# Optimization experiments

Measured on AMD Instinct MI355X. Metric: run time of the kernel, lower is better.

The kernel has to match this reference:

```python
import jax, jax.numpy as jnp
import numpy as np

ANNEAL = 0.01

def _tsig(x, temp=ANNEAL):
    # temperature sigmoid with +/-50 clipping as in the torch source
    return jax.nn.sigmoid(jnp.clip(x / temp, -50.0, 50.0))

def setup_inputs() -> dict:
    key = jax.random.key(0)
    k1, k2 = jax.random.split(key)
    N, D = 512, 512
    preds = jax.random.normal(k1, (N, D), dtype=jnp.float32)
    labels = jax.random.randint(k2, (N,), 0, 64, dtype=jnp.int64)
    return {"preds": preds, "labels": labels}

def reference(preds, labels):
    N = preds.shape[0]
    dtype = preds.dtype
    eye = jnp.eye(N, dtype=dtype)
    same = (labels[:, None] == labels[None, :]).astype(dtype)
    I_pos = same * (1.0 - eye)                      # positives excl. self
    sim_mat = preds @ preds.T                       # [N, N]
    # sim_diff[i, j, k] = sim_mat[i, k] - sim_mat[i, j]
    sim_sg = _tsig(sim_mat[:, None, :] - sim_mat[:, :, None]) * (1.0 - eye)[None, :, :]
    sim_all_rk = 1.0 + jnp.sum(sim_sg, axis=-1)     # [N, N]
    # sum_k sim_sg[i,j,k] * I_pos[i,k]
    pos_sum = jnp.einsum('ijk,ik->ij', sim_sg, I_pos)
    sim_pos_rk = eye + I_pos + I_pos * pos_sum      # [N, N]
    n_pos = jnp.sum(I_pos, axis=1) + 1.0            # [N]
    per_anchor = jnp.sum(sim_pos_rk / sim_all_rk, axis=1) / n_pos
    per_anchor = jnp.where(n_pos > 1.0, per_anchor, 0.0)  # skip anchors with no positives
    ap = jnp.sum(per_anchor) / N
    return 1.0 - ap
```

## Files before the change

kernel.cpp:

```cpp
#include <hip/hip_runtime.h>
#include <hip/hip_bf16.h>

#define NN 512

__global__ __launch_bounds__(256) void sap_gemm(const float* __restrict__ P,
                                                float* __restrict__ S) {
    __shared__ float As[32][33];
    __shared__ float Bs[32][33];
    const int t  = threadIdx.x;
    const int tx = t & 15, ty = t >> 4;
    const int i0 = blockIdx.y * 32, j0 = blockIdx.x * 32;

    float acc00 = 0.f, acc01 = 0.f, acc10 = 0.f, acc11 = 0.f;

    const int lr = t >> 3;
    const int lc = (t & 7) * 4;

    for (int kt = 0; kt < NN; kt += 32) {
        float4 a = *(const float4*)&P[(i0 + lr) * NN + kt + lc];
        float4 b = *(const float4*)&P[(j0 + lr) * NN + kt + lc];
        As[lr][lc + 0] = a.x; As[lr][lc + 1] = a.y;
        As[lr][lc + 2] = a.z; As[lr][lc + 3] = a.w;
        Bs[lr][lc + 0] = b.x; Bs[lr][lc + 1] = b.y;
        Bs[lr][lc + 2] = b.z; Bs[lr][lc + 3] = b.w;
        __syncthreads();
#pragma unroll
        for (int kk = 0; kk < 32; kk++) {
            float a0 = As[2 * ty][kk],     a1 = As[2 * ty + 1][kk];
            float b0 = Bs[2 * tx][kk],     b1 = Bs[2 * tx + 1][kk];
            acc00 += a0 * b0; acc01 += a0 * b1;
            acc10 += a1 * b0; acc11 += a1 * b1;
        }
        __syncthreads();
    }
    const int i = i0 + 2 * ty, j = j0 + 2 * tx;
    S[i * NN + j]           = acc00;
    S[i * NN + j + 1]       = acc01;
    S[(i + 1) * NN + j]     = acc10;
    S[(i + 1) * NN + j + 1] = acc11;
}

__global__ __launch_bounds__(256) void sap_rows(const float* __restrict__ S,
                                               const int* __restrict__ labels,
                                               float* __restrict__ per_anchor) {
    __shared__ float srow[NN];
    __shared__ float posf[NN];
    __shared__ int   poslist[NN];
    __shared__ int   npos_cnt;
    __shared__ float wave_part[4];

    const int i = blockIdx.x;
    const int t = threadIdx.x;
    if (t == 0) npos_cnt = 0;
    if (t < 4) wave_part[t] = 0.f;
    __syncthreads();

    const int li = labels[i];
    for (int k = t; k < NN; k += 256) {
        srow[k] = S[i * NN + k];
        bool p  = (labels[k] == li) && (k != i);
        posf[k] = p ? 1.f : 0.f;
        if (p) {
            int idx = atomicAdd(&npos_cnt, 1);
            poslist[idx] = k;
        }
    }
    __syncthreads();

    const int cnt = npos_cnt;
    if (cnt == 0) {
        if (t == 0) per_anchor[i] = 0.f;
        return;
    }

    const int wave = t >> 6, lane = t & 63;
    const float C1   = 100.0f * 1.44269504088896340736f;
    const float CLIP = 50.0f * 1.44269504088896340736f;

    float acc = 0.f;
    for (int idx = wave; idx <= cnt; idx += 4) {
        const int   j   = (idx == cnt) ? i : poslist[idx];
        const float sij = srow[j];
        float sum_all = 0.f, sum_pos = 0.f;
#pragma unroll
        for (int kk = 0; kk < 8; kk++) {
            const int   k  = lane + (kk << 6);
            float y = (sij - srow[k]) * C1;
            y = fminf(fmaxf(y, -CLIP), CLIP);
            float tt = 1.0f / (1.0f + exp2f(y));
            if (k == j) tt = 0.f;
            sum_all += tt;
            sum_pos += tt * posf[k];
        }
#pragma unroll
        for (int off = 32; off; off >>= 1) {
            sum_all += __shfl_down(sum_all, off);
            sum_pos += __shfl_down(sum_pos, off);
        }
        if (lane == 0) {
            const float den = 1.0f + sum_all;
            const float num = (j == i) ? 1.0f : (1.0f + sum_pos);
            acc += num / den;
        }
    }
    if (lane == 0) wave_part[wave] = acc;
    __syncthreads();
    if (t == 0) {
        float tot = wave_part[0] + wave_part[1] + wave_part[2] + wave_part[3];
        per_anchor[i] = tot / (float)(cnt + 1);
    }
}

__global__ __launch_bounds__(256) void sap_reduce(const float* __restrict__ per_anchor,
                                                  float* __restrict__ out) {
    __shared__ float sh[256];
    const int t = threadIdx.x;
    sh[t] = per_anchor[t] + per_anchor[t + 256];
    __syncthreads();
    for (int s = 128; s; s >>= 1) {
        if (t < s) sh[t] += sh[t + s];
        __syncthreads();
    }
    if (t == 0) out[0] = 1.0f - sh[0] / (float)NN;
}

extern "C" void kernel_launch(void* const* d_in, const int* in_sizes, int n_in,
                              void* d_out, int out_size, void* d_ws, size_t ws_size,
                              hipStream_t stream) {
    const float* preds  = (const float*)d_in[0];
    const int*   labels = (const int*)d_in[1];
    float* out = (float*)d_out;

    float* S          = (float*)d_ws;
    float* per_anchor = (float*)d_ws + NN * NN;

    dim3 ggrid(NN / 32, NN / 32);
    sap_gemm<<<ggrid, 256, 0, stream>>>(preds, S);
    sap_rows<<<NN, 256, 0, stream>>>(S, labels, per_anchor);
    sap_reduce<<<1, 256, 0, stream>>>(per_anchor, out);
}
```

Measured before the change: 79.62 us.

## Fuse final reduction into row kernel via atomics and retile GEMM with BK=64

Removes the separate reduce launch: each row block atomically adds its per-anchor value to a global accumulator, and the last block, found through an atomic counter, writes the loss. The GEMM now uses a K-tile of 64 stored transposed in shared memory, so each thread reads its operands as float2 and the kernel runs half as many tile loop iterations and barriers. This saves one kernel launch and some GEMM shared-memory traffic. In exchange, float atomics make the summation order nondeterministic, and the accumulator reset depends on the GEMM kernel running first.

New measurement: 83.22 us. 4.5% more time.

```diff
diff --git a/kernel.cpp b/kernel.cpp
--- a/kernel.cpp
+++ b/kernel.cpp
@@ -2,36 +2,47 @@
 #include <hip/hip_bf16.h>
 
 #define NN 512
+#define BK 64
 
 __global__ __launch_bounds__(256) void sap_gemm(const float* __restrict__ P,
-                                                float* __restrict__ S) {
-    __shared__ float As[32][33];
-    __shared__ float Bs[32][33];
+                                                float* __restrict__ S,
+                                                float* __restrict__ g_acc,
+                                                unsigned int* __restrict__ g_cnt) {
+    __shared__ float As[BK][34];
+    __shared__ float Bs[BK][34];
     const int t  = threadIdx.x;
     const int tx = t & 15, ty = t >> 4;
     const int i0 = blockIdx.y * 32, j0 = blockIdx.x * 32;
 
-    float acc00 = 0.f, acc01 = 0.f, acc10 = 0.f, acc11 = 0.f;
+    if (blockIdx.x == 0 && blockIdx.y == 0 && t == 0) { *g_acc = 0.f; *g_cnt = 0u; }
 
     const int lr = t >> 3;
     const int lc = (t & 7) * 4;
 
-    for (int kt = 0; kt < NN; kt += 32) {
-        float4 a = *(const float4*)&P[(i0 + lr) * NN + kt + lc];
-        float4 b = *(const float4*)&P[(j0 + lr) * NN + kt + lc];
-        As[lr][lc + 0] = a.x; As[lr][lc + 1] = a.y;
-        As[lr][lc + 2] = a.z; As[lr][lc + 3] = a.w;
-        Bs[lr][lc + 0] = b.x; Bs[lr][lc + 1] = b.y;
-        Bs[lr][lc + 2] = b.z; Bs[lr][lc + 3] = b.w;
+    float acc00 = 0.f, acc01 = 0.f, acc10 = 0.f, acc11 = 0.f;
+
+    for (int kt = 0; kt < NN; kt += BK) {
+        float4 a0 = *(const float4*)&P[(i0 + lr) * NN + kt + lc];
+        float4 a1 = *(const float4*)&P[(i0 + lr) * NN + kt + lc + 32];
+        float4 b0 = *(const float4*)&P[(j0 + lr) * NN + kt + lc];
+        float4 b1 = *(const float4*)&P[(j0 + lr) * NN + kt + lc + 32];
+        __syncthreads();
+        As[lc + 0][lr] = a0.x;  As[lc + 1][lr] = a0.y;
+        As[lc + 2][lr] = a0.z;  As[lc + 3][lr] = a0.w;
+        As[lc + 32][lr] = a1.x; As[lc + 33][lr] = a1.y;
+        As[lc + 34][lr] = a1.z; As[lc + 35][lr] = a1.w;
+        Bs[lc + 0][lr] = b0.x;  Bs[lc + 1][lr] = b0.y;
+        Bs[lc + 2][lr] = b0.z;  Bs[lc + 3][lr] = b0.w;
+        Bs[lc + 32][lr] = b1.x; Bs[lc + 33][lr] = b1.y;
+        Bs[lc + 34][lr] = b1.z; Bs[lc + 35][lr] = b1.w;
         __syncthreads();
 #pragma unroll
-        for (int kk = 0; kk < 32; kk++) {
-            float a0 = As[2 * ty][kk],     a1 = As[2 * ty + 1][kk];
-            float b0 = Bs[2 * tx][kk],     b1 = Bs[2 * tx + 1][kk];
-            acc00 += a0 * b0; acc01 += a0 * b1;
-            acc10 += a1 * b0; acc11 += a1 * b1;
+        for (int kk = 0; kk < BK; kk++) {
+            float2 av = *(const float2*)&As[kk][2 * ty];
+            float2 bv = *(const float2*)&Bs[kk][2 * tx];
+            acc00 += av.x * bv.x; acc01 += av.x * bv.y;
+            acc10 += av.y * bv.x; acc11 += av.y * bv.y;
         }
-        __syncthreads();
     }
     const int i = i0 + 2 * ty, j = j0 + 2 * tx;
     S[i * NN + j]           = acc00;
@@ -42,7 +53,9 @@
 
 __global__ __launch_bounds__(256) void sap_rows(const float* __restrict__ S,
                                                const int* __restrict__ labels,
-                                               float* __restrict__ per_anchor) {
+                                               float* __restrict__ g_acc,
+                                               unsigned int* __restrict__ g_cnt,
+                                               float* __restrict__ out) {
     __shared__ float srow[NN];
     __shared__ float posf[NN];
     __shared__ int   poslist[NN];
@@ -52,7 +65,6 @@
     const int i = blockIdx.x;
     const int t = threadIdx.x;
     if (t == 0) npos_cnt = 0;
-    if (t < 4) wave_part[t] = 0.f;
     __syncthreads();
 
     const int li = labels[i];
@@ -67,61 +79,55 @@
     }
     __syncthreads();
 
-    const int cnt = npos_cnt;
-    if (cnt == 0) {
-        if (t == 0) per_anchor[i] = 0.f;
-        return;
-    }
-
+    const int cnt  = npos_cnt;
     const int wave = t >> 6, lane = t & 63;
     const float C1   = 100.0f * 1.44269504088896340736f;
     const float CLIP = 50.0f * 1.44269504088896340736f;
 
     float acc = 0.f;
-    for (int idx = wave; idx <= cnt; idx += 4) {
-        const int   j   = (idx == cnt) ? i : poslist[idx];
-        const float sij = srow[j];
-        float sum_all = 0.f, sum_pos = 0.f;
+    if (cnt > 0) {
+        for (int idx = wave; idx <= cnt; idx += 4) {
+            const int   j   = (idx == cnt) ? i : poslist[idx];
+            const float sij = srow[j];
+            float sum_all = 0.f, sum_pos = 0.f;
 #pragma unroll
-        for (int kk = 0; kk < 8; kk++) {
-            const int   k  = lane + (kk << 6);
-            float y = (sij - srow[k]) * C1;
-            y = fminf(fmaxf(y, -CLIP), CLIP);
-            float tt = 1.0f / (1.0f + exp2f(y));
-            if (k == j) tt = 0.f;
-            sum_all += tt;
-            sum_pos += tt * posf[k];
-        }
+            for (int kk = 0; kk < 8; kk++) {
+                const int k = lane + (kk << 6);
+                float y = (sij - srow[k]) * C1;
+                y = fminf(fmaxf(y, -CLIP), CLIP);
+                float tt = 1.0f / (1.0f + exp2f(y));
+                if (k == j) tt = 0.f;
+                sum_all += tt;
+                sum_pos += tt * posf[k];
+            }
 #pragma unroll
-        for (int off = 32; off; off >>= 1) {
-            sum_all += __shfl_down(sum_all, off);
-            sum_pos += __shfl_down(sum_pos, off);
-        }
-        if (lane == 0) {
-            const float den = 1.0f + sum_all;
-            const float num = (j == i) ? 1.0f : (1.0f + sum_pos);
-            acc += num / den;
+            for (int off = 32; off; off >>= 1) {
+                sum_all += __shfl_down(sum_all, off);
+                sum_pos += __shfl_down(sum_pos, off);
+            }
+            if (lane == 0) {
+                const float den = 1.0f + sum_all;
+                const float num = (j == i) ? 1.0f : (1.0f + sum_pos);
+                acc += num / den;
+            }
         }
     }
     if (lane == 0) wave_part[wave] = acc;
     __syncthreads();
     if (t == 0) {
-        float tot = wave_part[0] + wave_part[1] + wave_part[2] + wave_part[3];
-        per_anchor[i] = tot / (float)(cnt + 1);
+        float block_val = 0.f;
+        if (cnt > 0) {
+            float tot = wave_part[0] + wave_part[1] + wave_part[2] + wave_part[3];
+            block_val = tot / (float)(cnt + 1);
+        }
+        atomicAdd(g_acc, block_val);
+        __threadfence();
+        unsigned int done = atomicAdd(g_cnt, 1u);
+        if (done == NN - 1) {
+            float total = atomicAdd(g_acc, 0.0f);
+            out[0] = 1.0f - total / (float)NN;
+        }
     }
-}
-
-__global__ __launch_bounds__(256) void sap_reduce(const float* __restrict__ per_anchor,
-                                                  float* __restrict__ out) {
-    __shared__ float sh[256];
-    const int t = threadIdx.x;
-    sh[t] = per_anchor[t] + per_anchor[t + 256];
-    __syncthreads();
-    for (int s = 128; s; s >>= 1) {
-        if (t < s) sh[t] += sh[t + s];
-        __syncthreads();
-    }
-    if (t == 0) out[0] = 1.0f - sh[0] / (float)NN;
 }
 
 extern "C" void kernel_launch(void* const* d_in, const int* in_sizes, int n_in,
@@ -131,11 +137,11 @@
     const int*   labels = (const int*)d_in[1];
     float* out = (float*)d_out;
 
-    float* S          = (float*)d_ws;
-    float* per_anchor = (float*)d_ws + NN * NN;
+    float*        S     = (float*)d_ws;
+    float*        g_acc = (float*)d_ws + NN * NN;
+    unsigned int* g_cnt = (unsigned int*)((float*)d_ws + NN * NN + 1);
 
     dim3 ggrid(NN / 32, NN / 32);
-    sap_gemm<<<ggrid, 256, 0, stream>>>(preds, S);
-    sap_rows<<<NN, 256, 0, stream>>>(S, labels, per_anchor);
-    sap_reduce<<<1, 256, 0, stream>>>(per_anchor, out);
+    sap_gemm<<<ggrid, 256, 0, stream>>>(preds, S, g_acc, g_cnt);
+    sap_rows<<<NN, 256, 0, stream>>>(S, labels, g_acc, g_cnt, out);
 }
```
